# Optimization experiments

Measured on AMD Instinct MI355X. Metric: run time of the kernel, lower is better.

Reference implementation:

```python
import jax, jax.numpy as jnp
import numpy as np

N_KERNELS = 11
INV_SQRT_2PI = 1.0 / np.sqrt(2.0 * 3.141592653589793)


def kernel_mus(n_kernels):
    l_mu = [1.0]
    if n_kernels == 1:
        return l_mu
    bin_size = 2.0 / (n_kernels - 1)
    l_mu.append(1 - bin_size / 2)
    for i in range(1, n_kernels - 1):
        l_mu.append(l_mu[i] - bin_size)
    return l_mu


def kernel_sigmas(n_kernels):
    bin_size = 2.0 / (n_kernels - 1)
    l_sigma = [0.0001]
    if n_kernels == 1:
        return l_sigma
    l_sigma += [0.5 * bin_size] * (n_kernels - 1)
    return l_sigma


MU = jnp.asarray(kernel_mus(N_KERNELS), dtype=jnp.float32)        # [K]
SIGMA = jnp.asarray(kernel_sigmas(N_KERNELS), dtype=jnp.float32)  # [K]


def setup_inputs() -> dict:
    key = jax.random.key(0)
    k1, k2, k3, k4 = jax.random.split(key, 4)
    B, Q, D, V, E = 512, 32, 256, 32000, 128
    return {
        "query_tokens": jax.random.randint(k1, (B, Q), 0, V),
        "doc_tokens": jax.random.randint(k2, (B, D), 0, V),
        "embedding": jax.random.normal(k3, (V, E), dtype=jnp.float32),
        "fc_weight": jax.random.normal(k4, (1, N_KERNELS), dtype=jnp.float32) * 0.3,
    }


def reference(query_tokens, doc_tokens, embedding, fc_weight):
    # embedding lookup + L2 normalization along feature dim
    q_emb = embedding[query_tokens]                                  # [B,Q,E]
    d_emb = embedding[doc_tokens]                                    # [B,D,E]
    q_n = q_emb / jnp.linalg.norm(q_emb, axis=-1, keepdims=True)
    d_n = d_emb / jnp.linalg.norm(d_emb, axis=-1, keepdims=True)

    # cosine similarity translation matrix [B,Q,D]
    tm = jnp.einsum("bqe,bde->bqd", q_n, d_n)

    # Gaussian kernel responses [B,Q,D,K] (vectorized over kernels)
    diff = tm[..., None] - MU                                        # [B,Q,D,K]
    kmat = jnp.exp(-(diff * diff) / (2.0 * SIGMA * SIGMA)) * INV_SQRT_2PI

    # masking: pad/OOV tokens (id 0) masked out
    q_mask = (query_tokens > 0).astype(jnp.float32)                  # [B,Q]
    d_mask = (doc_tokens > 0).astype(jnp.float32)                    # [B,D]
    kmat = kmat * q_mask[:, :, None, None] * d_mask[:, None, :, None]

    # kernel pooling: sum over doc, log, masked sum over query
    per_kernel_query = jnp.sum(kmat, axis=2)                         # [B,Q,K]
    log_pool = jnp.log(jnp.clip(per_kernel_query, 1e-10)) * q_mask[:, :, None]
    per_kernel = jnp.sum(log_pool, axis=1)                           # [B,K]

    # final linear (no bias) -> score per (query, document) pair
    return jnp.squeeze(per_kernel @ fc_weight.T, axis=-1)            # [B]
```

## Files before the change

kernel.cpp:

```cpp
#include <hip/hip_runtime.h>
#include <hip/hip_bf16.h>

#define EDIM  128
#define QN    32
#define DN    256
#define NK    11

typedef __attribute__((ext_vector_type(8))) short bf16x8;
typedef __attribute__((ext_vector_type(4))) float f32x4;

#define EXP2F(x) __builtin_amdgcn_exp2f(x)

template <int CTRL>
static __device__ inline float dpp_add(float x) {
    int y = __builtin_amdgcn_update_dpp(0, __float_as_int(x), CTRL, 0xF, 0xF, true);
    return x + __int_as_float(y);
}
static __device__ inline float sum16(float x) {
    x = dpp_add<0xB1>(x);
    x = dpp_add<0x4E>(x);
    x = dpp_add<0x124>(x);
    x = dpp_add<0x128>(x);
    return x;
}

static __device__ inline int swz(int r, int c) { return c ^ ((r & 7) << 4); }

static __device__ inline bf16x8 pack8(float4 a, float4 b) {
    union { bf16x8 v; __hip_bfloat16 h[8]; } u;
    u.h[0] = __float2bfloat16(a.x); u.h[1] = __float2bfloat16(a.y);
    u.h[2] = __float2bfloat16(a.z); u.h[3] = __float2bfloat16(a.w);
    u.h[4] = __float2bfloat16(b.x); u.h[5] = __float2bfloat16(b.y);
    u.h[6] = __float2bfloat16(b.z); u.h[7] = __float2bfloat16(b.w);
    return u.v;
}
static __device__ inline float sumsq8(float4 a, float4 b) {
    float s = a.x * a.x + a.y * a.y + a.z * a.z + a.w * a.w;
    s = fmaf(b.x, b.x, s); s = fmaf(b.y, b.y, s);
    s = fmaf(b.z, b.z, s); s = fmaf(b.w, b.w, s);
    return s;
}

__global__ __launch_bounds__(512, 4) void knrm_fused(const int* __restrict__ qtok,
                                                     const int* __restrict__ dtok,
                                                     const float* __restrict__ emb,
                                                     const float* __restrict__ fcw,
                                                     float* __restrict__ out) {
    __shared__ __align__(16) unsigned short dbuf[DN * EDIM];
    __shared__ __align__(16) unsigned short qbuf[QN * EDIM];
    __shared__ int   dtokS[DN];
    __shared__ int   qtokS[QN];
    __shared__ float invS[DN + QN];
    __shared__ float redS[8];

    const float C0 = 0.3989422804014327f;
    const float C1 = 7.30620157e-3f;
    const float C2 = 2.45119242e-6f;
    const float C3 = 1.50605972e-11f;
    const float C4 = 1.69484929e-18f;

    int b = blockIdx.x, tid = threadIdx.x;
    int w = tid >> 6, lane = tid & 63;
    int lr = lane & 15, lg = lane >> 4;

    if (tid < DN) dtokS[tid] = dtok[b * DN + tid];
    else if (tid < DN + QN) qtokS[tid - DN] = qtok[b * QN + (tid - DN)];
    __syncthreads();

    {
        int qr = (w << 2) + lg;
        int tok = qtokS[qr];
        const float4* src = (const float4*)(emb + (size_t)tok * EDIM) + lr * 2;
        float4 v0 = src[0], v1 = src[1];
        float tot = sum16(sumsq8(v0, v1));
        if (lr == 0) invS[DN + qr] = 1.0f / sqrtf(tot);
        *(bf16x8*)((char*)qbuf + qr * 256 + swz(qr, lr * 16)) = pack8(v0, v1);
    }
    #pragma unroll
    for (int it = 0; it < 4; ++it) {
        int r = (w << 4) + (it << 2) + lg;
        int tok = dtokS[r];
        const float4* src = (const float4*)(emb + (size_t)tok * EDIM) + lr * 2;
        float4 v0 = src[0], v1 = src[1];
        float tot = sum16(sumsq8(v0, v1));
        if (lr == 0) invS[r] = 1.0f / sqrtf(tot);
        *(bf16x8*)((char*)dbuf + r * 256 + swz(r, lr * 16)) = pack8(v0, v1);
    }
    __syncthreads();

    int qt = w & 1, ds = w >> 1;

    bf16x8 A0, A1, A2, A3;
    {
        int qr = (qt << 4) + lr;
        const char* qb = (const char*)qbuf + qr * 256;
        A0 = *(const bf16x8*)(qb + swz(qr, lg * 16));
        A1 = *(const bf16x8*)(qb + swz(qr, lg * 16 + 64));
        A2 = *(const bf16x8*)(qb + swz(qr, lg * 16 + 128));
        A3 = *(const bf16x8*)(qb + swz(qr, lg * 16 + 192));
    }
    int   qtr[4];
    float invq[4];
    #pragma unroll
    for (int r = 0; r < 4; ++r) {
        int qrow = (qt << 4) + (lg << 2) + r;
        qtr[r]  = qtokS[qrow];
        invq[r] = invS[DN + qrow];
    }

    float kacc[4][NK];
    #pragma unroll
    for (int r = 0; r < 4; ++r)
        #pragma unroll
        for (int k = 0; k < NK; ++k) kacc[r][k] = 0.0f;

    auto evalTile = [&](int t) {
        int dr = (t << 6) + (ds << 4) + lr;
        const char* db = (const char*)dbuf + dr * 256;
        bf16x8 B0 = *(const bf16x8*)(db + swz(dr, lg * 16));
        bf16x8 B1 = *(const bf16x8*)(db + swz(dr, lg * 16 + 64));
        bf16x8 B2 = *(const bf16x8*)(db + swz(dr, lg * 16 + 128));
        bf16x8 B3 = *(const bf16x8*)(db + swz(dr, lg * 16 + 192));
        int   tcur = dtokS[dr];
        float invd = invS[dr];

        f32x4 acc = {0.0f, 0.0f, 0.0f, 0.0f};
        acc = __builtin_amdgcn_mfma_f32_16x16x32_bf16(A0, B0, acc, 0, 0, 0);
        acc = __builtin_amdgcn_mfma_f32_16x16x32_bf16(A1, B1, acc, 0, 0, 0);
        acc = __builtin_amdgcn_mfma_f32_16x16x32_bf16(A2, B2, acc, 0, 0, 0);
        acc = __builtin_amdgcn_mfma_f32_16x16x32_bf16(A3, B3, acc, 0, 0, 0);

        bool dok = (tcur > 0);
        float mc = dok ? C0 : 0.0f;
        #pragma unroll
        for (int r = 0; r < 4; ++r) {
            float t2 = acc[r] * (invq[r] * invd);
            kacc[r][0] += (tcur == qtr[r]) ? mc : 0.0f;
            float d  = t2 - 0.1f;
            float g  = EXP2F(d * d * -72.1347520f);
            g = dok ? g : 0.0f;
            float Em = EXP2F(t2 * -28.8539008f);
            float Ep = EXP2F(t2 *  28.8539008f);
            float h = g;
            kacc[r][5]  += h * C0;
            h *= Em; kacc[r][6]  += h * C0;
            h *= Em; kacc[r][7]  += h * C1;
            h *= Em; kacc[r][8]  += h * C2;
            h *= Em; kacc[r][9]  += h * C3;
            h *= Em; kacc[r][10] += h * C4;
            h = g;
            h *= Ep; kacc[r][4]  += h * C1;
            h *= Ep; kacc[r][3]  += h * C2;
            h *= Ep; kacc[r][2]  += h * C3;
            h *= Ep; kacc[r][1]  += h * C4;
        }
    };

    #pragma unroll
    for (int it = 0; it < 4; ++it) {
        int r = 128 + (w << 4) + (it << 2) + lg;
        int tok = dtokS[r];
        const float4* src = (const float4*)(emb + (size_t)tok * EDIM) + lr * 2;
        float4 v0 = src[0], v1 = src[1];
        float tot = sum16(sumsq8(v0, v1));
        if (lr == 0) invS[r] = 1.0f / sqrtf(tot);
        *(bf16x8*)((char*)dbuf + r * 256 + swz(r, lr * 16)) = pack8(v0, v1);
    }
    evalTile(0);
    evalTile(1);
    __syncthreads();

    evalTile(2);
    evalTile(3);

    #pragma unroll
    for (int r = 0; r < 4; ++r)
        #pragma unroll
        for (int k = 0; k < NK; ++k) kacc[r][k] = sum16(kacc[r][k]);

    float* part = (float*)qbuf;
    if (lr == 0) {
        float* pw = part + w * (16 * NK) + (lg * 4) * NK;
        #pragma unroll
        for (int r = 0; r < 4; ++r)
            #pragma unroll
            for (int k = 0; k < NK; ++k)
                pw[r * NK + k] = kacc[r][k];
    }
    __syncthreads();

    float total = 0.0f;
    if (tid < QN * NK) {
        int q = tid / NK, k = tid - (tid / NK) * NK;
        int qt2 = q >> 4, row = q & 15;
        const float* pb = part + qt2 * (16 * NK) + row * NK + k;
        float v = pb[0] + pb[2 * 16 * NK] + pb[4 * 16 * NK] + pb[6 * 16 * NK];
        float m = (qtokS[q] > 0) ? 1.0f : 0.0f;
        total = m * fcw[k] * __logf(fmaxf(v, 1e-10f));
    }
    #pragma unroll
    for (int off = 32; off; off >>= 1) total += __shfl_xor(total, off);
    if (lane == 0) redS[w] = total;
    __syncthreads();
    if (tid == 0) {
        float s = 0.0f;
        #pragma unroll
        for (int i = 0; i < 8; ++i) s += redS[i];
        out[b] = s;
    }
}

extern "C" void kernel_launch(void* const* d_in, const int* in_sizes, int n_in,
                              void* d_out, int out_size, void* d_ws, size_t ws_size,
                              hipStream_t stream) {
    const int*   qtok = (const int*)d_in[0];
    const int*   dtok = (const int*)d_in[1];
    const float* emb  = (const float*)d_in[2];
    const float* fcw  = (const float*)d_in[3];
    float* out = (float*)d_out;

    int B = in_sizes[0] / QN;
    knrm_fused<<<B, 512, 0, stream>>>(qtok, dtok, emb, fcw, out);
}
```

Measured before the change: 21.21 us.

## Read tokens directly from global, prefetch all embeddings, pre-normalize before bf16

Drops the shared-memory token staging and its barrier: each thread loads the tokens it needs straight from global memory and issues every embedding row load up front, so all gathers are in flight together. Rows are normalized in registers before packing to bf16, which removes the per-element rescale by inverse norms after the MFMA. The old overlap of the second half of the doc gathers with the first tiles' compute is dropped in favour of one barrier before all compute. The cost is higher register pressure from holding nine rows' worth of float4 values per thread, and an extra barrier before the partial sums reuse qbuf.

```diff
diff --git a/kernel.cpp b/kernel.cpp
--- a/kernel.cpp
+++ b/kernel.cpp
@@ -48,9 +48,6 @@
                                                      float* __restrict__ out) {
     __shared__ __align__(16) unsigned short dbuf[DN * EDIM];
     __shared__ __align__(16) unsigned short qbuf[QN * EDIM];
-    __shared__ int   dtokS[DN];
-    __shared__ int   qtokS[QN];
-    __shared__ float invS[DN + QN];
     __shared__ float redS[8];
 
     const float C0 = 0.3989422804014327f;
@@ -62,33 +59,64 @@
     int b = blockIdx.x, tid = threadIdx.x;
     int w = tid >> 6, lane = tid & 63;
     int lr = lane & 15, lg = lane >> 4;
-
-    if (tid < DN) dtokS[tid] = dtok[b * DN + tid];
-    else if (tid < DN + QN) qtokS[tid - DN] = qtok[b * QN + (tid - DN)];
-    __syncthreads();
+    int qt = w & 1, ds = w >> 1;
+
+    const int* qtb = qtok + b * QN;
+    const int* dtb = dtok + b * DN;
+
+    int tq = qtb[(w << 2) + lg];
+    int tdA[4], tdB[4];
+    #pragma unroll
+    for (int it = 0; it < 4; ++it) {
+        tdA[it] = dtb[(w << 4) + (it << 2) + lg];
+        tdB[it] = dtb[128 + (w << 4) + (it << 2) + lg];
+    }
+    int tcurs[4], qtr[4];
+    #pragma unroll
+    for (int t = 0; t < 4; ++t) tcurs[t] = dtb[(t << 6) + (ds << 4) + lr];
+    #pragma unroll
+    for (int r = 0; r < 4; ++r) qtr[r] = qtb[(qt << 4) + (lg << 2) + r];
+
+    const float4* qsrc = (const float4*)(emb + (size_t)tq * EDIM) + lr * 2;
+    float4 qv0 = qsrc[0], qv1 = qsrc[1];
+    float4 av[4][2], bv[4][2];
+    #pragma unroll
+    for (int it = 0; it < 4; ++it) {
+        const float4* s0 = (const float4*)(emb + (size_t)tdA[it] * EDIM) + lr * 2;
+        av[it][0] = s0[0]; av[it][1] = s0[1];
+    }
+    #pragma unroll
+    for (int it = 0; it < 4; ++it) {
+        const float4* s1 = (const float4*)(emb + (size_t)tdB[it] * EDIM) + lr * 2;
+        bv[it][0] = s1[0]; bv[it][1] = s1[1];
+    }
 
     {
         int qr = (w << 2) + lg;
-        int tok = qtokS[qr];
-        const float4* src = (const float4*)(emb + (size_t)tok * EDIM) + lr * 2;
-        float4 v0 = src[0], v1 = src[1];
-        float tot = sum16(sumsq8(v0, v1));
-        if (lr == 0) invS[DN + qr] = 1.0f / sqrtf(tot);
-        *(bf16x8*)((char*)qbuf + qr * 256 + swz(qr, lr * 16)) = pack8(v0, v1);
+        float inv = 1.0f / sqrtf(sum16(sumsq8(qv0, qv1)));
+        qv0.x *= inv; qv0.y *= inv; qv0.z *= inv; qv0.w *= inv;
+        qv1.x *= inv; qv1.y *= inv; qv1.z *= inv; qv1.w *= inv;
+        *(bf16x8*)((char*)qbuf + qr * 256 + swz(qr, lr * 16)) = pack8(qv0, qv1);
     }
     #pragma unroll
     for (int it = 0; it < 4; ++it) {
         int r = (w << 4) + (it << 2) + lg;
-        int tok = dtokS[r];
-        const float4* src = (const float4*)(emb + (size_t)tok * EDIM) + lr * 2;
-        float4 v0 = src[0], v1 = src[1];
-        float tot = sum16(sumsq8(v0, v1));
-        if (lr == 0) invS[r] = 1.0f / sqrtf(tot);
+        float inv = 1.0f / sqrtf(sum16(sumsq8(av[it][0], av[it][1])));
+        float4 v0 = av[it][0], v1 = av[it][1];
+        v0.x *= inv; v0.y *= inv; v0.z *= inv; v0.w *= inv;
+        v1.x *= inv; v1.y *= inv; v1.z *= inv; v1.w *= inv;
         *(bf16x8*)((char*)dbuf + r * 256 + swz(r, lr * 16)) = pack8(v0, v1);
     }
-    __syncthreads();
-
-    int qt = w & 1, ds = w >> 1;
+    #pragma unroll
+    for (int it = 0; it < 4; ++it) {
+        int r = 128 + (w << 4) + (it << 2) + lg;
+        float inv = 1.0f / sqrtf(sum16(sumsq8(bv[it][0], bv[it][1])));
+        float4 v0 = bv[it][0], v1 = bv[it][1];
+        v0.x *= inv; v0.y *= inv; v0.z *= inv; v0.w *= inv;
+        v1.x *= inv; v1.y *= inv; v1.z *= inv; v1.w *= inv;
+        *(bf16x8*)((char*)dbuf + r * 256 + swz(r, lr * 16)) = pack8(v0, v1);
+    }
+    __syncthreads();
 
     bf16x8 A0, A1, A2, A3;
     {
@@ -99,14 +127,6 @@
         A2 = *(const bf16x8*)(qb + swz(qr, lg * 16 + 128));
         A3 = *(const bf16x8*)(qb + swz(qr, lg * 16 + 192));
     }
-    int   qtr[4];
-    float invq[4];
-    #pragma unroll
-    for (int r = 0; r < 4; ++r) {
-        int qrow = (qt << 4) + (lg << 2) + r;
-        qtr[r]  = qtokS[qrow];
-        invq[r] = invS[DN + qrow];
-    }
 
     float kacc[4][NK];
     #pragma unroll
@@ -114,15 +134,15 @@
         #pragma unroll
         for (int k = 0; k < NK; ++k) kacc[r][k] = 0.0f;
 
-    auto evalTile = [&](int t) {
+    #pragma unroll
+    for (int t = 0; t < 4; ++t) {
         int dr = (t << 6) + (ds << 4) + lr;
         const char* db = (const char*)dbuf + dr * 256;
         bf16x8 B0 = *(const bf16x8*)(db + swz(dr, lg * 16));
         bf16x8 B1 = *(const bf16x8*)(db + swz(dr, lg * 16 + 64));
         bf16x8 B2 = *(const bf16x8*)(db + swz(dr, lg * 16 + 128));
         bf16x8 B3 = *(const bf16x8*)(db + swz(dr, lg * 16 + 192));
-        int   tcur = dtokS[dr];
-        float invd = invS[dr];
+        int tcur = tcurs[t];
 
         f32x4 acc = {0.0f, 0.0f, 0.0f, 0.0f};
         acc = __builtin_amdgcn_mfma_f32_16x16x32_bf16(A0, B0, acc, 0, 0, 0);
@@ -134,7 +154,7 @@
         float mc = dok ? C0 : 0.0f;
         #pragma unroll
         for (int r = 0; r < 4; ++r) {
-            float t2 = acc[r] * (invq[r] * invd);
+            float t2 = acc[r];
             kacc[r][0] += (tcur == qtr[r]) ? mc : 0.0f;
             float d  = t2 - 0.1f;
             float g  = EXP2F(d * d * -72.1347520f);
@@ -154,33 +174,16 @@
             h *= Ep; kacc[r][2]  += h * C3;
             h *= Ep; kacc[r][1]  += h * C4;
         }
-    };
-
-    #pragma unroll
-    for (int it = 0; it < 4; ++it) {
-        int r = 128 + (w << 4) + (it << 2) + lg;
-        int tok = dtokS[r];
-        const float4* src = (const float4*)(emb + (size_t)tok * EDIM) + lr * 2;
-        float4 v0 = src[0], v1 = src[1];
-        float tot = sum16(sumsq8(v0, v1));
-        if (lr == 0) invS[r] = 1.0f / sqrtf(tot);
-        *(bf16x8*)((char*)dbuf + r * 256 + swz(r, lr * 16)) = pack8(v0, v1);
-    }
-    evalTile(0);
-    evalTile(1);
-    __syncthreads();
-
-    evalTile(2);
-    evalTile(3);
-
+    }
+
+    __syncthreads();
+    float* part = (float*)qbuf;
     #pragma unroll
     for (int r = 0; r < 4; ++r)
         #pragma unroll
         for (int k = 0; k < NK; ++k) kacc[r][k] = sum16(kacc[r][k]);
-
-    float* part = (float*)qbuf;
     if (lr == 0) {
-        float* pw = part + w * (16 * NK) + (lg * 4) * NK;
+        float* pw = part + w * (16 * NK) + (lg << 2) * NK;
         #pragma unroll
         for (int r = 0; r < 4; ++r)
             #pragma unroll
@@ -195,7 +198,7 @@
         int qt2 = q >> 4, row = q & 15;
         const float* pb = part + qt2 * (16 * NK) + row * NK + k;
         float v = pb[0] + pb[2 * 16 * NK] + pb[4 * 16 * NK] + pb[6 * 16 * NK];
-        float m = (qtokS[q] > 0) ? 1.0f : 0.0f;
+        float m = (qtb[q] > 0) ? 1.0f : 0.0f;
         total = m * fcw[k] * __logf(fmaxf(v, 1e-10f));
     }
     #pragma unroll
```

After: 21.86 us. 1.03x slower.
